# Kernel optimization log

Hardware: AMD Instinct MI355X
Metric: run time of the kernel (lower is better)

Reference implementation:

```python
import jax, jax.numpy as jnp
import numpy as np

MAXLEN = 128  # cfg.maxlen: max instances per image; mask IDs in [0, MAXLEN], 0 = background


def setup_inputs() -> dict:
    key = jax.random.key(0)
    ks = jax.random.split(key, 8)
    B, C, h, w = 32, 512, 64, 64
    Hm = Wm = 512
    n_cls, att_h = 19, 512
    s = 0.02
    return {
        "x": jax.random.normal(ks[0], (B, C, h, w), dtype=jnp.float32),
        "mask": jax.random.randint(ks[1], (B, Hm, Wm), 0, MAXLEN + 1, dtype=jnp.int64),
        "target": jax.random.uniform(ks[2], (B, n_cls), dtype=jnp.float32),
        "Wa1": jax.random.normal(ks[3], (C, att_h), dtype=jnp.float32) * s,
        "ba1": jnp.zeros((att_h,), jnp.float32),
        "Wa2": jax.random.normal(ks[4], (att_h, 1), dtype=jnp.float32) * s,
        "ba2": jnp.zeros((1,), jnp.float32),
        "Wh": jax.random.normal(ks[5], (C, n_cls), dtype=jnp.float32) * s,
        "bh": jnp.zeros((n_cls,), jnp.float32),
    }


def _nearest_downsample(mask, h, w):
    # torch F.interpolate(mode='nearest'): out[i] = in[floor(i * in/out)]
    B, Hm, Wm = mask.shape
    ri = (jnp.arange(h) * Hm) // h
    ci = (jnp.arange(w) * Wm) // w
    return mask[:, ri[:, None], ci[None, :]]  # [B,h,w]


def reference(x, mask, target, Wa1, ba1, Wa2, ba2, Wh, bh):
    B, C, h, w = x.shape
    m2 = _nearest_downsample(mask, h, w)           # [B,h,w] int
    ids = m2.reshape(B, h * w)                     # [B,P]
    feats = x.reshape(B, C, h * w).transpose(0, 2, 1)  # [B,P,C]

    def seg(f, i):
        s = jax.ops.segment_sum(f, i, num_segments=MAXLEN + 1)          # [M+1,C]
        c = jax.ops.segment_sum(jnp.ones(i.shape, f.dtype), i, num_segments=MAXLEN + 1)
        return s, c

    sums, counts = jax.vmap(seg)(feats, ids)       # [B,M+1,C], [B,M+1]
    sums, counts = sums[:, 1:], counts[:, 1:]      # drop background id 0
    # per-instance masked mean; absent ids -> zero row (matches zero-padding)
    means = jnp.where(counts[..., None] > 0,
                      sums / jnp.maximum(counts, 1.0)[..., None], 0.0)  # [B,M,C]

    att = jnp.maximum(means @ Wa1 + ba1, 0.0) @ Wa2 + ba2  # [B,M,1]
    att = jax.nn.softmax(att, axis=1)                       # softmax over instances
    cls = means @ Wh + bh                                   # [B,M,n_cls]
    logits = jnp.sum(cls * att, axis=1)                     # [B,n_cls]

    # BCEWithLogitsLoss, mean reduction (numerically stable)
    loss = jnp.mean(jnp.maximum(logits, 0.0) - logits * target
                    + jnp.log1p(jnp.exp(-jnp.abs(logits))))
    return logits, loss
```

## Files before the change

### kernel.cpp

```cpp
#include <hip/hip_runtime.h>
#include <math.h>

#define NB 32
#define NC 512
#define HW 4096
#define NSEG 128
#define NCLS 19

#define OFF_COUNTS 8388608
#define OFF_ALOG   8404992
#define OFF_WLOSS  8421376
#define OFF_IDS    8421504
#define ZERO_F4    525312

__global__ __launch_bounds__(256) void k_zero(float4* __restrict__ p) {
  int i = blockIdx.x * 1024 + threadIdx.x;
  float4 z = make_float4(0.f, 0.f, 0.f, 0.f);
#pragma unroll
  for (int j = 0; j < 4; ++j) p[i + j * 256] = z;
}

__global__ __launch_bounds__(256) void k_ids_counts(const int* __restrict__ mask,
                                                    unsigned char* __restrict__ ids,
                                                    float* __restrict__ counts) {
  int rq = blockIdx.x, b = blockIdx.y;
  int t = threadIdx.x;
  __shared__ int cnt[NSEG + 1];
  if (t < NSEG + 1) cnt[t] = 0;
  __syncthreads();
  const int* mb = mask + (size_t)b * 262144;
  int p0 = rq * 1024 + t * 4;
  uchar4 wv;
  unsigned char* wp = (unsigned char*)&wv;
#pragma unroll
  for (int j = 0; j < 4; ++j) {
    int p = p0 + j;
    int i = p >> 6, jj = p & 63;
    int id = mb[i * 4096 + jj * 8];
    wp[j] = (unsigned char)id;
    atomicAdd(&cnt[id], 1);
  }
  *(uchar4*)(ids + (size_t)b * HW + p0) = wv;
  __syncthreads();
  if (t < NSEG) atomicAdd(&counts[b * NSEG + t], (float)cnt[t + 1]);
}

__global__ __launch_bounds__(256) void k_segmeans(const float* __restrict__ x,
                                                  const unsigned char* __restrict__ ids,
                                                  float* __restrict__ sums) {
  int cc = blockIdx.x, pq = blockIdx.y, b = blockIdx.z;
  int t = threadIdx.x;
  int w = t >> 6;
  int lane = t & 63;
  __shared__ float bins[129 * 65];
  __shared__ float tile[64 * 65];
  __shared__ unsigned char lids[1024];

  for (int i = t; i < 129 * 65; i += 256) bins[i] = 0.f;
  ((uchar4*)lids)[t] = ((const uchar4*)(ids + (size_t)b * HW + pq * 1024))[t];

  int l16 = t & 15;
  int r0 = t >> 4;
  const float* xbase = x + ((size_t)(b * NC + cc * 64)) * HW + pq * 1024 + 4 * l16;

  float4 v[4], vn[4];
#pragma unroll
  for (int rr = 0; rr < 4; ++rr)
    v[rr] = *(const float4*)(xbase + (size_t)(r0 + rr * 16) * HW);
  __syncthreads();

  for (int ti = 0; ti < 16; ++ti) {
#pragma unroll
    for (int rr = 0; rr < 4; ++rr) {
      int c = r0 + rr * 16;
      int p = 4 * l16;
      tile[(p + 0) * 65 + c] = v[rr].x;
      tile[(p + 1) * 65 + c] = v[rr].y;
      tile[(p + 2) * 65 + c] = v[rr].z;
      tile[(p + 3) * 65 + c] = v[rr].w;
    }
    __syncthreads();
    if (ti < 15) {
#pragma unroll
      for (int rr = 0; rr < 4; ++rr)
        vn[rr] = *(const float4*)(xbase + (size_t)(r0 + rr * 16) * HW + (ti + 1) * 64);
    }
    int pbase = ti * 64;
#pragma unroll 4
    for (int j = 0; j < 64; ++j) {
      int s = lids[pbase + j];
      if ((s & 3) == w) {
        bins[s * 65 + lane] += tile[j * 65 + lane];
      }
    }
    __syncthreads();
#pragma unroll
    for (int rr = 0; rr < 4; ++rr) v[rr] = vn[rr];
  }

  for (int i = t; i < NSEG * 64; i += 256) {
    int s = (i >> 6) + 1, c = i & 63;
    float vv = bins[s * 65 + c];
    if (vv != 0.f) atomicAdd(&sums[((size_t)b * NSEG + (s - 1)) * NC + cc * 64 + c], vv);
  }
}

__global__ __launch_bounds__(256) void k_att(const float* __restrict__ sums,
                                             const float* __restrict__ counts,
                                             const float* __restrict__ Wa1,
                                             const float* __restrict__ ba1,
                                             const float* __restrict__ Wa2,
                                             const float* __restrict__ ba2,
                                             float* __restrict__ alog) {
  int st = blockIdx.x, b = blockIdx.y;
  int t = threadIdx.x;
  __shared__ float mt[8 * 512];
  __shared__ float red[4][8];
  const float4* m4 = (const float4*)(sums + ((size_t)b * NSEG + st * 8) * NC);
  float4* mt4 = (float4*)mt;
#pragma unroll
  for (int i = 0; i < 4; ++i) {
    int idx = i * 256 + t;
    int r = idx >> 7;
    float cn = counts[b * NSEG + st * 8 + r];
    float inv = cn > 0.f ? 1.f / cn : 0.f;
    float4 mv = m4[idx];
    mv.x *= inv; mv.y *= inv; mv.z *= inv; mv.w *= inv;
    mt4[idx] = mv;
  }
  __syncthreads();

  float2 acc[8];
#pragma unroll
  for (int r = 0; r < 8; ++r) acc[r] = make_float2(0.f, 0.f);

  float wc0[4], wc1[4], wn0[4], wn1[4];
#pragma unroll
  for (int kk = 0; kk < 4; ++kk) {
    wc0[kk] = Wa1[(size_t)kk * 512 + t];
    wc1[kk] = Wa1[(size_t)kk * 512 + t + 256];
  }
  for (int k4 = 0; k4 < 128; ++k4) {
    if (k4 < 127) {
      int k = (k4 + 1) * 4;
#pragma unroll
      for (int kk = 0; kk < 4; ++kk) {
        wn0[kk] = Wa1[(size_t)(k + kk) * 512 + t];
        wn1[kk] = Wa1[(size_t)(k + kk) * 512 + t + 256];
      }
    }
    int k = k4 * 4;
#pragma unroll
    for (int r = 0; r < 8; ++r) {
      float4 m = *(const float4*)&mt[r * 512 + k];
      acc[r].x = fmaf(m.x, wc0[0], fmaf(m.y, wc0[1], fmaf(m.z, wc0[2], fmaf(m.w, wc0[3], acc[r].x))));
      acc[r].y = fmaf(m.x, wc1[0], fmaf(m.y, wc1[1], fmaf(m.z, wc1[2], fmaf(m.w, wc1[3], acc[r].y))));
    }
#pragma unroll
    for (int kk = 0; kk < 4; ++kk) { wc0[kk] = wn0[kk]; wc1[kk] = wn1[kk]; }
  }

  float b1a = ba1[t], b1b = ba1[t + 256];
  float w2a = Wa2[t], w2b = Wa2[t + 256];
  int lane = t & 63, wid = t >> 6;
#pragma unroll
  for (int r = 0; r < 8; ++r) {
    float v = fmaxf(acc[r].x + b1a, 0.f) * w2a + fmaxf(acc[r].y + b1b, 0.f) * w2b;
#pragma unroll
    for (int off = 32; off > 0; off >>= 1) v += __shfl_down(v, off, 64);
    if (lane == 0) red[wid][r] = v;
  }
  __syncthreads();
  if (t < 8) {
    alog[b * NSEG + st * 8 + t] = red[0][t] + red[1][t] + red[2][t] + red[3][t] + ba2[0];
  }
}

__global__ __launch_bounds__(256) void k_head(const float* __restrict__ sums,
                                              const float* __restrict__ counts,
                                              const float* __restrict__ alog,
                                              const float* __restrict__ Wh,
                                              const float* __restrict__ bh,
                                              const float* __restrict__ target,
                                              float* __restrict__ out,
                                              float* __restrict__ wloss) {
  int b = blockIdx.x, t = threadIdx.x;
  __shared__ float att[NSEG];
  __shared__ float wm[NC];
  __shared__ float sred[4];
  __shared__ float sval;
  __shared__ float part[8][20];
  __shared__ float lg[NCLS];
  int lane = t & 63, wid = t >> 6;

  float l = (t < NSEG) ? alog[b * NSEG + t] : -INFINITY;
  float v = l;
#pragma unroll
  for (int off = 32; off > 0; off >>= 1) v = fmaxf(v, __shfl_down(v, off, 64));
  if (lane == 0) sred[wid] = v;
  __syncthreads();
  if (t == 0) sval = fmaxf(fmaxf(sred[0], sred[1]), fmaxf(sred[2], sred[3]));
  __syncthreads();
  float mx = sval;
  float e = (t < NSEG) ? expf(l - mx) : 0.f;
  v = e;
#pragma unroll
  for (int off = 32; off > 0; off >>= 1) v += __shfl_down(v, off, 64);
  if (lane == 0) sred[wid] = v;
  __syncthreads();
  if (t == 0) sval = sred[0] + sred[1] + sred[2] + sred[3];
  __syncthreads();
  float isum = 1.f / sval;
  if (t < NSEG) {
    float cn = counts[b * NSEG + t];
    float inv = cn > 0.f ? 1.f / cn : 0.f;
    att[t] = e * isum * inv;
  }
  __syncthreads();

  const float* mb = sums + (size_t)b * NSEG * NC;
  {
    float s0 = 0.f, s1 = 0.f, s2 = 0.f, s3 = 0.f;
#pragma unroll 4
    for (int sg = 0; sg < NSEG; sg += 2) {
      float a0 = att[sg], a1 = att[sg + 1];
      const float* rp = mb + (size_t)sg * NC;
      s0 = fmaf(a0, rp[t], s0);
      s1 = fmaf(a0, rp[t + 256], s1);
      s2 = fmaf(a1, rp[NC + t], s2);
      s3 = fmaf(a1, rp[NC + t + 256], s3);
    }
    wm[t] = s0 + s2;
    wm[t + 256] = s1 + s3;
  }
  __syncthreads();

  if (t < 152) {
    int g = t / NCLS, cls = t - g * NCLS;
    float p = 0.f;
#pragma unroll 8
    for (int i = 0; i < 64; ++i) {
      int k = g + 8 * i;
      p = fmaf(wm[k], Wh[k * NCLS + cls], p);
    }
    part[g][cls] = p;
  }
  __syncthreads();
  if (t < NCLS) {
    float s = bh[t];
#pragma unroll
    for (int g = 0; g < 8; ++g) s += part[g][t];
    lg[t] = s;
    out[b * NCLS + t] = s;
  }
  __syncthreads();
  if (t < 64) {
    float term = 0.f;
    if (t < NCLS) {
      float xg = lg[t];
      term = fmaxf(xg, 0.f) - xg * target[b * NCLS + t] + log1pf(expf(-fabsf(xg)));
    }
#pragma unroll
    for (int off = 32; off > 0; off >>= 1) term += __shfl_down(term, off, 64);
    if (t == 0) wloss[b] = term;
  }
}

__global__ void k_loss(const float* __restrict__ wloss, float* __restrict__ out) {
  int t = threadIdx.x;
  float v = (t < NB) ? wloss[t] : 0.f;
#pragma unroll
  for (int off = 32; off > 0; off >>= 1) v += __shfl_down(v, off, 64);
  if (t == 0) out[NB * NCLS] = v * (1.f / (NB * NCLS));
}

extern "C" void kernel_launch(void* const* d_in, const int* in_sizes, int n_in,
                              void* d_out, int out_size, void* d_ws, size_t ws_size,
                              hipStream_t stream) {
  const float* x = (const float*)d_in[0];
  const int* mask = (const int*)d_in[1];
  const float* target = (const float*)d_in[2];
  const float* Wa1 = (const float*)d_in[3];
  const float* ba1 = (const float*)d_in[4];
  const float* Wa2 = (const float*)d_in[5];
  const float* ba2 = (const float*)d_in[6];
  const float* Wh = (const float*)d_in[7];
  const float* bh = (const float*)d_in[8];
  float* out = (float*)d_out;

  char* ws = (char*)d_ws;
  float* sums = (float*)ws;
  float* counts = (float*)(ws + OFF_COUNTS);
  float* alog = (float*)(ws + OFF_ALOG);
  float* wloss = (float*)(ws + OFF_WLOSS);
  unsigned char* ids = (unsigned char*)(ws + OFF_IDS);

  k_zero<<<513, 256, 0, stream>>>((float4*)ws);
  k_ids_counts<<<dim3(4, NB), 256, 0, stream>>>(mask, ids, counts);
  k_segmeans<<<dim3(8, 4, NB), 256, 0, stream>>>(x, ids, sums);
  k_att<<<dim3(16, NB), 256, 0, stream>>>(sums, counts, Wa1, ba1, Wa2, ba2, alog);
  k_head<<<NB, 256, 0, stream>>>(sums, counts, alog, Wh, bh, target, out, wloss);
  k_loss<<<1, 64, 0, stream>>>(wloss, out);
}
```

Baseline: 552.9 us.

## Split segment-sum pixels across waves with LDS atomics; widen attention MLP blocks

In the segment-mean kernel, each wave now handles a disjoint 16-pixel slice of the tile and accumulates into shared bins with LDS atomicAdd. Before, all four waves scanned every pixel and kept only the segments they owned by id modulo 4. This removes the 4x redundant scan and the divergent branch, at the cost of atomic contention when lanes in different waves hit the same segment. The attention kernel now launches 512 threads per block, one hidden unit per thread, which halves per-thread work and registers and widens the reduction to eight waves.

Measured after the change: 712.6 us. 28.9% more time.

```diff
diff --git a/kernel.cpp b/kernel.cpp
--- a/kernel.cpp
+++ b/kernel.cpp
@@ -85,13 +85,11 @@
       for (int rr = 0; rr < 4; ++rr)
         vn[rr] = *(const float4*)(xbase + (size_t)(r0 + rr * 16) * HW + (ti + 1) * 64);
     }
-    int pbase = ti * 64;
+    int pbase = ti * 64 + w * 16;
 #pragma unroll 4
-    for (int j = 0; j < 64; ++j) {
-      int s = lids[pbase + j];
-      if ((s & 3) == w) {
-        bins[s * 65 + lane] += tile[j * 65 + lane];
-      }
+    for (int jj = 0; jj < 16; ++jj) {
+      int s = lids[pbase + jj];
+      atomicAdd(&bins[s * 65 + lane], tile[(w * 16 + jj) * 65 + lane]);
     }
     __syncthreads();
 #pragma unroll
@@ -105,7 +103,7 @@
   }
 }
 
-__global__ __launch_bounds__(256) void k_att(const float* __restrict__ sums,
+__global__ __launch_bounds__(512) void k_att(const float* __restrict__ sums,
                                              const float* __restrict__ counts,
                                              const float* __restrict__ Wa1,
                                              const float* __restrict__ ba1,
@@ -115,12 +113,12 @@
   int st = blockIdx.x, b = blockIdx.y;
   int t = threadIdx.x;
   __shared__ float mt[8 * 512];
-  __shared__ float red[4][8];
+  __shared__ float red[8][8];
   const float4* m4 = (const float4*)(sums + ((size_t)b * NSEG + st * 8) * NC);
   float4* mt4 = (float4*)mt;
 #pragma unroll
-  for (int i = 0; i < 4; ++i) {
-    int idx = i * 256 + t;
+  for (int i = 0; i < 2; ++i) {
+    int idx = i * 512 + t;
     int r = idx >> 7;
     float cn = counts[b * NSEG + st * 8 + r];
     float inv = cn > 0.f ? 1.f / cn : 0.f;
@@ -130,49 +128,46 @@
   }
   __syncthreads();
 
-  float2 acc[8];
-#pragma unroll
-  for (int r = 0; r < 8; ++r) acc[r] = make_float2(0.f, 0.f);
-
-  float wc0[4], wc1[4], wn0[4], wn1[4];
-#pragma unroll
-  for (int kk = 0; kk < 4; ++kk) {
-    wc0[kk] = Wa1[(size_t)kk * 512 + t];
-    wc1[kk] = Wa1[(size_t)kk * 512 + t + 256];
-  }
+  float acc[8];
+#pragma unroll
+  for (int r = 0; r < 8; ++r) acc[r] = 0.f;
+
+  float wc[4], wn[4];
+#pragma unroll
+  for (int kk = 0; kk < 4; ++kk) wc[kk] = Wa1[(size_t)kk * 512 + t];
+
   for (int k4 = 0; k4 < 128; ++k4) {
     if (k4 < 127) {
       int k = (k4 + 1) * 4;
 #pragma unroll
-      for (int kk = 0; kk < 4; ++kk) {
-        wn0[kk] = Wa1[(size_t)(k + kk) * 512 + t];
-        wn1[kk] = Wa1[(size_t)(k + kk) * 512 + t + 256];
-      }
+      for (int kk = 0; kk < 4; ++kk) wn[kk] = Wa1[(size_t)(k + kk) * 512 + t];
     }
     int k = k4 * 4;
 #pragma unroll
     for (int r = 0; r < 8; ++r) {
       float4 m = *(const float4*)&mt[r * 512 + k];
-      acc[r].x = fmaf(m.x, wc0[0], fmaf(m.y, wc0[1], fmaf(m.z, wc0[2], fmaf(m.w, wc0[3], acc[r].x))));
-      acc[r].y = fmaf(m.x, wc1[0], fmaf(m.y, wc1[1], fmaf(m.z, wc1[2], fmaf(m.w, wc1[3], acc[r].y))));
-    }
-#pragma unroll
-    for (int kk = 0; kk < 4; ++kk) { wc0[kk] = wn0[kk]; wc1[kk] = wn1[kk]; }
-  }
-
-  float b1a = ba1[t], b1b = ba1[t + 256];
-  float w2a = Wa2[t], w2b = Wa2[t + 256];
+      acc[r] = fmaf(m.x, wc[0], fmaf(m.y, wc[1], fmaf(m.z, wc[2], fmaf(m.w, wc[3], acc[r]))));
+    }
+#pragma unroll
+    for (int kk = 0; kk < 4; ++kk) wc[kk] = wn[kk];
+  }
+
+  float b1 = ba1[t];
+  float w2 = Wa2[t];
   int lane = t & 63, wid = t >> 6;
 #pragma unroll
   for (int r = 0; r < 8; ++r) {
-    float v = fmaxf(acc[r].x + b1a, 0.f) * w2a + fmaxf(acc[r].y + b1b, 0.f) * w2b;
+    float v = fmaxf(acc[r] + b1, 0.f) * w2;
 #pragma unroll
     for (int off = 32; off > 0; off >>= 1) v += __shfl_down(v, off, 64);
     if (lane == 0) red[wid][r] = v;
   }
   __syncthreads();
   if (t < 8) {
-    alog[b * NSEG + st * 8 + t] = red[0][t] + red[1][t] + red[2][t] + red[3][t] + ba2[0];
+    float s = ba2[0];
+#pragma unroll
+    for (int g = 0; g < 8; ++g) s += red[g][t];
+    alog[b * NSEG + st * 8 + t] = s;
   }
 }
 
@@ -298,7 +293,7 @@
   k_zero<<<513, 256, 0, stream>>>((float4*)ws);
   k_ids_counts<<<dim3(4, NB), 256, 0, stream>>>(mask, ids, counts);
   k_segmeans<<<dim3(8, 4, NB), 256, 0, stream>>>(x, ids, sums);
-  k_att<<<dim3(16, NB), 256, 0, stream>>>(sums, counts, Wa1, ba1, Wa2, ba2, alog);
+  k_att<<<dim3(16, NB), 512, 0, stream>>>(sums, counts, Wa1, ba1, Wa2, ba2, alog);
   k_head<<<NB, 256, 0, stream>>>(sums, counts, alog, Wh, bh, target, out, wloss);
   k_loss<<<1, 64, 0, stream>>>(wloss, out);
 }
```
